# Performance work log

Measured on AMD Instinct MI355X. Metric: run time of the kernel, lower is better.

## Reference

```python
import jax, jax.numpy as jnp
import numpy as np

B, N, C, H = 4, 1025, 768, 12
KEEP_RATIO = 0.25
BETA = 1.0


def setup_inputs() -> dict:
    key = jax.random.key(0)
    k1, k2, k3, k4, k5 = jax.random.split(key, 5)
    x = jax.random.normal(k1, (B, N, C), dtype=jnp.float32)
    ucb_count_score = jax.random.uniform(k2, (H, N), dtype=jnp.float32)
    W_qkv = jax.random.normal(k3, (C, 3 * C), dtype=jnp.float32) * 0.02
    W_proj = jax.random.normal(k4, (C, C), dtype=jnp.float32) * 0.02
    b_proj = jax.random.normal(k5, (C,), dtype=jnp.float32) * 0.02
    return {"x": x, "ucb_count_score": ucb_count_score, "W_qkv": W_qkv,
            "W_proj": W_proj, "b_proj": b_proj, "counter": 100, "ucb_enabled": 1}


def reference(x, ucb_count_score, W_qkv, W_proj, b_proj, counter, ucb_enabled):
    Bn, Nn, Cn = x.shape
    Dh = Cn // H
    scale = Dh ** -0.5
    # qkv projection (no bias, qkv_bias=False)
    qkv = (x @ W_qkv).reshape(Bn, Nn, 3, H, Dh)
    q = jnp.transpose(qkv[:, :, 0], (0, 2, 1, 3))  # [B,H,N,Dh]
    k = jnp.transpose(qkv[:, :, 1], (0, 2, 1, 3))
    v = jnp.transpose(qkv[:, :, 2], (0, 2, 1, 3))
    attn_probs = jax.nn.softmax(jnp.einsum('bhnd,bhmd->bhnm', q, k) * scale, axis=-1)

    if ucb_enabled and counter > 50:
        # UCB pruning path (exclude_cls=True, keep_ratio set)
        total_patches = Nn - 1
        k_sel = max(1, int(total_patches * KEEP_RATIO))
        patch_scores = attn_probs[:, :, :, 1:].mean(axis=2)  # [B,H,N-1]
        expl = BETA * jnp.sqrt(jnp.log(counter + 1.0) / (ucb_count_score[:, 1:] + 1e-6))  # [H,N-1]
        global_ucb = (patch_scores + expl[None]).mean(axis=1)  # [B,N-1]
        _, sel = jax.lax.top_k(global_ucb, k_sel)  # [B,k]
        tok = sel + 1  # shift for CLS
        # keep[b,j] = 1 if token j is CLS or selected in batch b
        keep = jnp.zeros((Bn, Nn), dtype=attn_probs.dtype)
        keep = keep.at[jnp.arange(Bn)[:, None], tok].set(1.0).at[:, 0].set(1.0)
        # mask[b,h,i,j] = keep[b,i] OR keep[b,j]
        mask = jnp.maximum(keep[:, None, :, None], keep[:, None, None, :])
        pruned = attn_probs * mask
        pruned = pruned / (pruned.sum(axis=-1, keepdims=True) + 1e-8)
        context = jnp.einsum('bhnm,bhmd->bhnd', pruned, v)
        cnt = jnp.zeros((Nn,), dtype=jnp.float32).at[tok.reshape(-1)].add(1.0) / Bn
        score_delta = jnp.broadcast_to(cnt[None, :], ucb_count_score.shape)
    else:
        context = jnp.einsum('bhnm,bhmd->bhnd', attn_probs, v)
        score_delta = None

    out = context.transpose(0, 2, 1, 3).reshape(Bn, Nn, Cn) @ W_proj + b_proj
    return out, score_delta
```

## Files before the change

kernel.cpp:

```cpp
#include <hip/hip_runtime.h>
#include <hip/hip_bf16.h>
#include <math.h>

#define Bb 4
#define Nn 1025
#define Cc 768
#define Hh 12
#define BH (Bb*Hh)
#define M_ROWS 4100
#define KSEL 256
#define JP 1152
#define IT_TILES 68
#define NIB 17
#define NIB32 33
#define NSW 9
#define MT16 264
#define KC24 24
#define JT16 72
#define JT32 36
#define STR4 292
#define NPART 396
#define NSCORE 1024
#define QSCALE 0.18033688011112042f

#define CAST_X_BLK 1584
#define CAST_WQKV_BLK 864
#define CAST_WPROJ_BLK 288

typedef __attribute__((ext_vector_type(8))) short short8;
typedef __attribute__((ext_vector_type(4))) short short4s;
typedef __attribute__((ext_vector_type(4))) float floatx4;
typedef __attribute__((ext_vector_type(4))) unsigned uintx4;

static __device__ inline unsigned short f2bf(float v) {
    __hip_bfloat16 b = __float2bfloat16(v);
    return *reinterpret_cast<unsigned short*>(&b);
}
static __device__ inline float fexp2(float x) {
    return __builtin_amdgcn_exp2f(x);
}
static __device__ inline unsigned pkbf(float lo, float hi) {
    union { float f; unsigned u; } a, b;
    a.f = lo; b.f = hi;
    return (a.u >> 16) | (b.u & 0xffff0000u);
}

static __device__ inline void async16(const unsigned short* g, unsigned short* l) {
    __builtin_amdgcn_global_load_lds(
        (const __attribute__((address_space(1))) unsigned int*)g,
        (__attribute__((address_space(3))) unsigned int*)l, 16, 0, 0);
}

__global__ __launch_bounds__(256)
void cast_all(const float* __restrict__ x, const float* __restrict__ Wqkv,
              const float* __restrict__ Wproj,
              unsigned short* __restrict__ xA, unsigned short* __restrict__ WB,
              unsigned short* __restrict__ WpB)
{
    int blk = blockIdx.x;
    int tid = threadIdx.x;
    if (blk < CAST_X_BLK) {
        int s = blk * 256 + tid;
        int ml = s & 15, q = (s >> 4) & 3;
        int t2 = s >> 6;
        int mt = t2 % MT16, kc = t2 / MT16;
        int m = mt * 16 + ml, k = kc * 32 + q * 8;
        uint4 pk = {0u, 0u, 0u, 0u};
        if (m < M_ROWS) {
            float4 a = *(const float4*)&x[(size_t)m * 768 + k];
            float4 b2 = *(const float4*)&x[(size_t)m * 768 + k + 4];
            pk.x = (unsigned)f2bf(a.x)  | ((unsigned)f2bf(a.y)  << 16);
            pk.y = (unsigned)f2bf(a.z)  | ((unsigned)f2bf(a.w)  << 16);
            pk.z = (unsigned)f2bf(b2.x) | ((unsigned)f2bf(b2.y) << 16);
            pk.w = (unsigned)f2bf(b2.z) | ((unsigned)f2bf(b2.w) << 16);
        }
        *(uint4*)&xA[(size_t)s * 8] = pk;
        return;
    }
    const float* W;
    unsigned short* WO;
    int N, NT, s;
    if (blk < CAST_X_BLK + CAST_WQKV_BLK) {
        W = Wqkv; WO = WB; N = 2304; NT = 144;
        s = (blk - CAST_X_BLK) * 256 + tid;
    } else {
        W = Wproj; WO = WpB; N = 768; NT = 48;
        s = (blk - CAST_X_BLK - CAST_WQKV_BLK) * 256 + tid;
    }
    int nl = s & 15, q = (s >> 4) & 3;
    int t2 = s >> 6;
    int nt = t2 % NT, kc = t2 / NT;
    int n = nt * 16 + nl, k = kc * 32 + q * 8;
    unsigned hv[8];
#pragma unroll
    for (int e = 0; e < 8; ++e)
        hv[e] = f2bf(W[(size_t)(k + e) * N + n]);
    uint4 pk;
    pk.x = hv[0] | (hv[1] << 16);
    pk.y = hv[2] | (hv[3] << 16);
    pk.z = hv[4] | (hv[5] << 16);
    pk.w = hv[6] | (hv[7] << 16);
    *(uint4*)&WO[(size_t)s * 8] = pk;
}

template<int NT, int MODE>
__global__ __launch_bounds__(256, 3)
void gemm_mfma(const unsigned short* __restrict__ Af,
               const unsigned short* __restrict__ Bf,
               int Nt16,
               unsigned short* __restrict__ qB, unsigned short* __restrict__ kF,
               unsigned short* __restrict__ vF,
               float* __restrict__ outp, const float* __restrict__ bias)
{
    __shared__ __align__(16) unsigned short ldsA[4096];
    __shared__ __align__(16) unsigned short ldsB[NT * 1024];
    const int tid = threadIdx.x;
    const int ln = tid & 63, w = tid >> 6;
    const int wm = w >> 1, wn = w & 1;
    const int mb = blockIdx.x, nb = blockIdx.y;

    floatx4 acc[4][NT];
#pragma unroll
    for (int mt = 0; mt < 4; ++mt)
#pragma unroll
        for (int nt = 0; nt < NT; ++nt)
            acc[mt][nt] = (floatx4){0.f, 0.f, 0.f, 0.f};

    for (int kc = 0; kc < KC24; ++kc) {
        const unsigned short* gA = Af + ((size_t)(kc * MT16 + mb * 8)) * 512;
        const unsigned short* gB = Bf + ((size_t)(kc * Nt16 + nb * (NT * 2))) * 512;
        async16(gA + (size_t)(w * 128 + ln) * 8,      &ldsA[w * 1024]);
        async16(gA + (size_t)(w * 128 + 64 + ln) * 8, &ldsA[w * 1024 + 512]);
        if (NT == 4) {
            async16(gB + (size_t)(w * 128 + ln) * 8,      &ldsB[w * 1024]);
            async16(gB + (size_t)(w * 128 + 64 + ln) * 8, &ldsB[w * 1024 + 512]);
        } else {
            async16(gB + (size_t)(w * 64 + ln) * 8, &ldsB[w * 512]);
        }
        __syncthreads();

        short8 Am[4], Bn[NT];
#pragma unroll
        for (int mt = 0; mt < 4; ++mt)
            Am[mt] = *(const short8*)&ldsA[((wm * 4 + mt) * 64 + ln) * 8];
#pragma unroll
        for (int nt = 0; nt < NT; ++nt)
            Bn[nt] = *(const short8*)&ldsB[((wn * NT + nt) * 64 + ln) * 8];
#pragma unroll
        for (int mt = 0; mt < 4; ++mt)
#pragma unroll
            for (int nt = 0; nt < NT; ++nt)
                acc[mt][nt] = __builtin_amdgcn_mfma_f32_16x16x32_bf16(
                    Am[mt], Bn[nt], acc[mt][nt], 0, 0, 0);
        __syncthreads();
    }

    const int q = ln >> 4, l15 = ln & 15;
    if (MODE == 1) {
#pragma unroll
        for (int nt = 0; nt < NT; ++nt) {
            int gn = nb * (NT * 32) + wn * (NT * 16) + nt * 16 + l15;
            float bv = bias[gn];
#pragma unroll
            for (int mt = 0; mt < 4; ++mt) {
                int gmb = mb * 128 + wm * 64 + mt * 16 + q * 4;
#pragma unroll
                for (int r = 0; r < 4; ++r) {
                    int gm = gmb + r;
                    if (gm < M_ROWS)
                        outp[(size_t)gm * 768 + gn] = acc[mt][nt][r] + bv;
                }
            }
        }
    } else {
#pragma unroll
        for (int nt = 0; nt < NT; ++nt) {
            int gn = nb * (NT * 32) + wn * (NT * 16) + nt * 16 + l15;
            int s = (gn >= 1536) ? 2 : (gn >= 768 ? 1 : 0);
            int rr = gn - s * Cc;
            int h = rr >> 6, d = rr & 63;
#pragma unroll
            for (int mt = 0; mt < 4; ++mt) {
                int gmb = mb * 128 + wm * 64 + mt * 16 + q * 4;
#pragma unroll
                for (int r = 0; r < 4; ++r) {
                    int gm = gmb + r;
                    if (gm >= M_ROWS) continue;
                    int b = gm / Nn;
                    int n = gm - b * Nn;
                    int bh = b * Hh + h;
                    float val = acc[mt][nt][r];
                    if (s == 0) {
                        int idx = (((bh * IT_TILES + (n >> 4)) * 2 + (d >> 5)) * 512)
                                  + ((((d & 31) >> 3) * 16 + (n & 15)) * 8) + (d & 7);
                        qB[idx] = f2bf(val * QSCALE);
                    } else if (s == 1) {
                        size_t idx = ((((size_t)bh * JT16 + (n >> 4)) * 2 + (d >> 5)) * 64
                                      + ((d >> 3) & 3) * 16 + (n & 15)) * 8 + (d & 7);
                        kF[idx] = f2bf(val);
                    } else {
                        size_t idx = ((((size_t)bh * JT32 + (n >> 5)) * 4 + (d >> 4)) * 64
                                      + ((n >> 3) & 3) * 16 + (d & 15)) * 8 + (n & 7);
                        vF[idx] = f2bf(val);
                    }
                }
            }
        }
    }
}

__global__ __launch_bounds__(256, 4)
void attn_colsum_mfma(const unsigned short* __restrict__ qB,
                      const unsigned short* __restrict__ kF,
                      float* __restrict__ colsum_part)
{
    __shared__ unsigned int expS8[32 * STR4];
    __shared__ float red16[16][32];
    __shared__ float linv[32];

    const int blk = blockIdx.x;
    const int x8 = blk & 7, g = blk >> 3;
    const int bh = x8 * 6 + (g % 6);
    const int ib = g / 6;
    const int tid = threadIdx.x;
    const int ws = tid >> 6;
    const int ln = tid & 63;
    const int i16 = ln & 15, q = ln >> 4;

    const unsigned short* kBase = kF + (size_t)bh * JT16 * 1024;

    short8 Qf[2][2];
#pragma unroll
    for (int it = 0; it < 2; ++it)
#pragma unroll
        for (int kc = 0; kc < 2; ++kc)
            Qf[it][kc] = *(const short8*)&qB[(((size_t)bh * IT_TILES + ib * 2 + it) * 2 + kc) * 512 + ln * 8];

    float lacc[2][2] = {{0.f, 0.f}, {0.f, 0.f}};

    short8 Kc[2][2], Kn[2][2];
#pragma unroll
    for (int jt = 0; jt < 2; ++jt)
#pragma unroll
        for (int kc = 0; kc < 2; ++kc)
            Kc[jt][kc] = *(const short8*)&kBase[(((ws * 2 + jt) * 2 + kc) * 64 + ln) * 8];

    for (int sw = 0; sw < NSW; ++sw) {
        if (sw + 1 < NSW) {
#pragma unroll
            for (int jt = 0; jt < 2; ++jt)
#pragma unroll
                for (int kc = 0; kc < 2; ++kc)
                    Kn[jt][kc] = *(const short8*)&kBase[((((sw + 1) * 8 + ws * 2 + jt) * 2 + kc) * 64 + ln) * 8];
        }

        floatx4 S[2][2];
#pragma unroll
        for (int it = 0; it < 2; ++it)
#pragma unroll
            for (int jt = 0; jt < 2; ++jt) {
                S[it][jt] = (floatx4){0.f, 0.f, 0.f, 0.f};
#pragma unroll
                for (int kc = 0; kc < 2; ++kc)
                    S[it][jt] = __builtin_amdgcn_mfma_f32_16x16x32_bf16(Kc[jt][kc], Qf[it][kc], S[it][jt], 0, 0, 0);
            }

        const int jbase0 = sw * 128 + ws * 32 + q * 4;
#pragma unroll
        for (int it = 0; it < 2; ++it) {
            const int irow = it * 16 + i16;
#pragma unroll
            for (int jt = 0; jt < 2; ++jt) {
                int jbase = jbase0 + jt * 16;
                float p[4];
#pragma unroll
                for (int r = 0; r < 4; ++r) {
                    float vld = (jbase + r < Nn) ? 1.f : 0.f;
                    p[r] = fexp2(S[it][jt][r]) * vld;
                }
                lacc[it][jt] += (p[0] + p[1]) + (p[2] + p[3]);
                unsigned u = (unsigned)__builtin_amdgcn_cvt_pk_fp8_f32(p[0], p[1], 0, false);
                u = (unsigned)__builtin_amdgcn_cvt_pk_fp8_f32(p[2], p[3], (int)u, true);
                expS8[irow * STR4 + (jbase >> 2)] = u;
            }
        }
#pragma unroll
        for (int jt = 0; jt < 2; ++jt)
#pragma unroll
            for (int kc = 0; kc < 2; ++kc)
                Kc[jt][kc] = Kn[jt][kc];
    }

    __syncthreads();
#pragma unroll
    for (int it = 0; it < 2; ++it)
        red16[ws * 4 + q][it * 16 + i16] = lacc[it][0] + lacc[it][1];
    __syncthreads();
    if (tid < 32) {
        float s = 0.f;
#pragma unroll
        for (int t = 0; t < 16; ++t) s += red16[t][tid];
        int gi = ib * 32 + tid;
        linv[tid] = (gi < Nn) ? 1.f / s : 0.f;
    }
    __syncthreads();

    float* prow = colsum_part + (size_t)(bh * NIB32 + ib) * JP;
    for (int grp = tid; grp < 288; grp += 256) {
        float a0 = 0.f, a1 = 0.f, a2 = 0.f, a3 = 0.f;
#pragma unroll 8
        for (int i = 0; i < 32; ++i) {
            unsigned v = expS8[i * STR4 + grp];
            float li = linv[i];
            a0 += __builtin_amdgcn_cvt_f32_fp8(v, 0) * li;
            a1 += __builtin_amdgcn_cvt_f32_fp8(v, 1) * li;
            a2 += __builtin_amdgcn_cvt_f32_fp8(v, 2) * li;
            a3 += __builtin_amdgcn_cvt_f32_fp8(v, 3) * li;
        }
        float4 o = {a0, a1, a2, a3};
        *(float4*)&prow[grp * 4] = o;
    }
}

__global__ __launch_bounds__(256)
void colsum_reduce(const float* __restrict__ colsum_part,
                   const float* __restrict__ ucb_score,
                   const int* __restrict__ counter_p,
                   float* __restrict__ scoreF)
{
    const int b = blockIdx.x, jc = blockIdx.y;
    const int tid = threadIdx.x;
    const int j32 = tid & 31, grp = tid >> 5;
    const int t = jc * 32 + j32 + 1;
    __shared__ float red[8][32];

    const float* pb = colsum_part + (size_t)b * NPART * JP + t;
    float a0 = 0.f, a1 = 0.f;
    int r = grp;
    for (; r + 8 < NPART; r += 16) {
        a0 += pb[(size_t)r * JP];
        a1 += pb[(size_t)(r + 8) * JP];
    }
    for (; r < NPART; r += 8) a0 += pb[(size_t)r * JP];
    red[grp][j32] = a0 + a1;
    __syncthreads();

    if (tid < 32) {
        float cs = 0.f;
#pragma unroll
        for (int g = 0; g < 8; ++g) cs += red[g][tid];
        int tt = jc * 32 + tid + 1;
        float lc = logf((float)(*counter_p) + 1.0f);
        float s = cs * (1.0f / (float)Nn);
#pragma unroll
        for (int h = 0; h < Hh; ++h)
            s += sqrtf(lc / (ucb_score[h * Nn + tt] + 1e-6f));
        s *= (1.0f / (float)Hh);
        scoreF[b * NSCORE + tt - 1] = s;
    }
}

__global__ __launch_bounds__(1024)
void ucb_topk(const float* __restrict__ scoreF,
              float* __restrict__ keepP, float* __restrict__ cnt_b)
{
    const int b = blockIdx.x;
    const int tid = threadIdx.x;
    const int w = tid >> 6, ln = tid & 63;
    __shared__ int hist[8192];
    __shared__ int wtot[16];
    __shared__ unsigned ckey[1024];
    __shared__ int cidx[1024];
    __shared__ int s_tb, s_rem, ccount;

    for (int tpos = tid; tpos < JP; tpos += 1024) {
        keepP[b * JP + tpos] = 0.f;
        cnt_b[b * JP + tpos] = 0.f;
    }

    const unsigned key = __float_as_uint(scoreF[b * NSCORE + tid]);

    for (int tpos = tid; tpos < 8192; tpos += 1024) hist[tpos] = 0;
    if (tid == 0) ccount = 0;
    __syncthreads();
    atomicAdd(&hist[key >> 18], 1);
    __syncthreads();

    int part = 0;
#pragma unroll
    for (int q2 = 0; q2 < 8; ++q2) part += hist[tid * 8 + q2];
    int v = part;
#pragma unroll
    for (int off = 1; off < 64; off <<= 1) {
        int tv = __shfl_down(v, off);
        if (ln + off < 64) v += tv;
    }
    if (ln == 0) wtot[w] = v;
    __syncthreads();
    int woff = 0;
    for (int w2 = w + 1; w2 < 16; ++w2) woff += wtot[w2];
    int cum_above = v + woff - part;
    for (int q2 = 7; q2 >= 0; --q2) {
        int c = hist[tid * 8 + q2];
        if (cum_above < KSEL && cum_above + c >= KSEL) {
            s_tb = tid * 8 + q2;
            s_rem = KSEL - cum_above;
        }
        cum_above += c;
    }
    __syncthreads();

    const int tb = s_tb, rem = s_rem;
    const int mybin = (int)(key >> 18);
    bool sel = mybin > tb;
    if (mybin == tb) {
        int p = atomicAdd(&ccount, 1);
        ckey[p] = key; cidx[p] = tid;
    }
    __syncthreads();
    if (mybin == tb) {
        int rr = 0;
        const int cc = ccount;
        for (int c = 0; c < cc; ++c) {
            unsigned kc2 = ckey[c]; int ic = cidx[c];
            if (kc2 > key || (kc2 == key && ic < tid)) ++rr;
        }
        sel = rr < rem;
    }
    if (sel) {
        int tok = tid + 1;
        keepP[b * JP + tok] = 1.f;
        cnt_b[b * JP + tok] = 1.0f / (float)Bb;
    }
    if (tid == 0) keepP[b * JP + 0] = 1.f;
}

__global__ __launch_bounds__(256, 2)
void attn_ctx_mfma(const unsigned short* __restrict__ qB,
                   const unsigned short* __restrict__ kF,
                   const unsigned short* __restrict__ vF,
                   const float* __restrict__ keepP, const float* __restrict__ cnt_b,
                   unsigned short* __restrict__ ctxA, float* __restrict__ out2)
{
    __shared__ __align__(16) char smem[25856];
    float* keeps = (float*)smem;
    float* red16 = (float*)(smem + 4608);
    float* dinv  = (float*)(smem + 8704);
    float* redC  = (float*)(smem + 8960);

    const int blk = blockIdx.x;
    const int x8 = blk & 7, g = blk >> 3;
    const int bh = x8 * 6 + (g % 6);
    const int ib = g / 6;
    const int b = bh / Hh, h = bh % Hh;
    const int tid = threadIdx.x;
    const int ws = tid >> 6;
    const int ln = tid & 63;
    const int i16 = ln & 15, q = ln >> 4;

    {
        int t = blk * 256 + tid;
        if (t < Hh * Nn) {
            int n = t % Nn;
            out2[t] = cnt_b[0 * JP + n] + cnt_b[1 * JP + n]
                    + cnt_b[2 * JP + n] + cnt_b[3 * JP + n];
        }
    }

    for (int t = tid; t < JP; t += 256) keeps[t] = keepP[b * JP + t];

    const unsigned short* kBase = kF + (size_t)bh * JT16 * 1024;
    const unsigned short* vBase = vF + (size_t)bh * JT32 * 2048;

    short8 Qf[4][2];
#pragma unroll
    for (int it = 0; it < 4; ++it)
#pragma unroll
        for (int kc = 0; kc < 2; ++kc)
            Qf[it][kc] = *(const short8*)&qB[(((size_t)bh * IT_TILES + ib * 4 + it) * 2 + kc) * 512 + ln * 8];

    __syncthreads();

    float keepi[4];
#pragma unroll
    for (int it = 0; it < 4; ++it)
        keepi[it] = keeps[(ib * 4 + it) * 16 + i16];

    floatx4 ctxacc[4][4];
#pragma unroll
    for (int it = 0; it < 4; ++it)
#pragma unroll
        for (int dt = 0; dt < 4; ++dt)
            ctxacc[it][dt] = (floatx4){0.f, 0.f, 0.f, 0.f};
    float dsacc[4] = {0.f, 0.f, 0.f, 0.f};

    short8 Kc[2][2], Kn[2][2];
    short8 Vc8[4], Vn8[4];
#pragma unroll
    for (int jt = 0; jt < 2; ++jt)
#pragma unroll
        for (int kc = 0; kc < 2; ++kc)
            Kc[jt][kc] = *(const short8*)&kBase[(((ws * 2 + jt) * 2 + kc) * 64 + ln) * 8];
#pragma unroll
    for (int dt = 0; dt < 4; ++dt)
        Vc8[dt] = *(const short8*)&vBase[(((size_t)ws * 4 + dt) * 64 + ln) * 8];

    for (int sw = 0; sw < NSW; ++sw) {
        if (sw + 1 < NSW) {
#pragma unroll
            for (int jt = 0; jt < 2; ++jt)
#pragma unroll
                for (int kc = 0; kc < 2; ++kc)
                    Kn[jt][kc] = *(const short8*)&kBase[((((sw + 1) * 8 + ws * 2 + jt) * 2 + kc) * 64 + ln) * 8];
#pragma unroll
            for (int dt = 0; dt < 4; ++dt)
                Vn8[dt] = *(const short8*)&vBase[((((size_t)(sw + 1) * 4 + ws) * 4 + dt) * 64 + ln) * 8];
        }

        float kjv[2][4], vld[2][4];
#pragma unroll
        for (int jt = 0; jt < 2; ++jt)
#pragma unroll
            for (int r = 0; r < 4; ++r) {
                int jj = sw * 128 + ws * 32 + jt * 16 + q * 4 + r;
                vld[jt][r] = (jj < Nn) ? 1.f : 0.f;
                kjv[jt][r] = keeps[jj];
            }

#pragma unroll
        for (int it = 0; it < 4; ++it) {
            floatx4 S[2];
#pragma unroll
            for (int jt = 0; jt < 2; ++jt) {
                S[jt] = (floatx4){0.f, 0.f, 0.f, 0.f};
#pragma unroll
                for (int kc = 0; kc < 2; ++kc)
                    S[jt] = __builtin_amdgcn_mfma_f32_16x16x32_bf16(Kc[jt][kc], Qf[it][kc], S[jt], 0, 0, 0);
            }
            bool rk = keepi[it] > 0.5f;
            float p[2][4];
#pragma unroll
            for (int jt = 0; jt < 2; ++jt)
#pragma unroll
                for (int r = 0; r < 4; ++r) {
                    float w = rk ? vld[jt][r] : kjv[jt][r];
                    p[jt][r] = fexp2(S[jt][r]) * w;
                    dsacc[it] += p[jt][r];
                }
            unsigned Au = pkbf(p[0][0], p[0][1]);
            unsigned Bu = pkbf(p[0][2], p[0][3]);
            unsigned Cu = pkbf(p[1][0], p[1][1]);
            unsigned Du = pkbf(p[1][2], p[1][3]);
            asm("v_permlane32_swap_b32 %0, %1" : "+v"(Au), "+v"(Cu));
            asm("v_permlane32_swap_b32 %0, %1" : "+v"(Bu), "+v"(Du));
            asm("v_permlane16_swap_b32 %0, %1" : "+v"(Au), "+v"(Cu));
            asm("v_permlane16_swap_b32 %0, %1" : "+v"(Bu), "+v"(Du));
            short8 Wf = __builtin_bit_cast(short8, (uintx4){Au, Bu, Cu, Du});
#pragma unroll
            for (int dt = 0; dt < 4; ++dt)
                ctxacc[it][dt] = __builtin_amdgcn_mfma_f32_16x16x32_bf16(
                    Wf, Vc8[dt], ctxacc[it][dt], 0, 0, 0);
        }

#pragma unroll
        for (int jt = 0; jt < 2; ++jt)
#pragma unroll
            for (int kc = 0; kc < 2; ++kc)
                Kc[jt][kc] = Kn[jt][kc];
#pragma unroll
        for (int dt = 0; dt < 4; ++dt)
            Vc8[dt] = Vn8[dt];
    }

    __syncthreads();
#pragma unroll
    for (int it = 0; it < 4; ++it) red16[(ws * 4 + q) * 64 + it * 16 + i16] = dsacc[it];
    __syncthreads();
    if (tid < 64) {
        float s = 0.f;
#pragma unroll
        for (int t = 0; t < 16; ++t) s += red16[t * 64 + tid];
        dinv[tid] = 1.f / (s + 1e-8f);
    }
    for (int w = 0; w < 4; ++w) {
        __syncthreads();
        if (ws == w) {
#pragma unroll
            for (int it = 0; it < 4; ++it)
#pragma unroll
                for (int dt = 0; dt < 4; ++dt)
#pragma unroll
                    for (int r = 0; r < 4; ++r) {
                        int i = it * 16 + q * 4 + r;
                        int d = dt * 16 + i16;
                        float v = ctxacc[it][dt][r];
                        redC[i * 66 + d] = (w == 0) ? v : (redC[i * 66 + d] + v);
                    }
        }
    }
    __syncthreads();
#pragma unroll
    for (int rep = 0; rep < 2; ++rep) {
        int s2 = tid + rep * 256;
        int i = s2 >> 3, dc = s2 & 7;
        int gi = ib * 64 + i;
        if (gi < Nn) {
            int m = b * Nn + gi;
            float dv = dinv[i];
            const float* src = &redC[i * 66 + dc * 8];
            uint4 pk;
            pk.x = (unsigned)f2bf(src[0] * dv) | ((unsigned)f2bf(src[1] * dv) << 16);
            pk.y = (unsigned)f2bf(src[2] * dv) | ((unsigned)f2bf(src[3] * dv) << 16);
            pk.z = (unsigned)f2bf(src[4] * dv) | ((unsigned)f2bf(src[5] * dv) << 16);
            pk.w = (unsigned)f2bf(src[6] * dv) | ((unsigned)f2bf(src[7] * dv) << 16);
            int kc2 = h * 2 + (dc >> 2);
            int q2 = dc & 3;
            size_t idx = (((size_t)(kc2 * MT16 + (m >> 4))) * 64 + q2 * 16 + (m & 15)) * 8;
            *(uint4*)&ctxA[idx] = pk;
        }
    }
}

extern "C" void kernel_launch(void* const* d_in, const int* in_sizes, int n_in,
                              void* d_out, int out_size, void* d_ws, size_t ws_size,
                              hipStream_t stream) {
    const float* x     = (const float*)d_in[0];
    const float* ucb   = (const float*)d_in[1];
    const float* Wqkv  = (const float*)d_in[2];
    const float* Wproj = (const float*)d_in[3];
    const float* bproj = (const float*)d_in[4];
    const int*   counter = (const int*)d_in[5];

    unsigned short* qB = (unsigned short*)d_ws;
    unsigned short* kF = qB + 3342336;
    unsigned short* vF = kF + 3538944;
    float* keepP    = (float*)(vF + 3538944);
    float* cnt_b    = keepP + 4608;
    unsigned short* ctxA = (unsigned short*)(cnt_b + 4608);
    unsigned short* xA   = ctxA + 3244032;
    unsigned short* WB   = xA + 3244032;
    unsigned short* WpB  = WB + 1769472;
    float* colsum_part = (float*)(WpB + 589824);
    float* scoreF = colsum_part + 1824768;

    float* out  = (float*)d_out;
    float* out2 = out + 3148800;

    cast_all<<<dim3(CAST_X_BLK + CAST_WQKV_BLK + CAST_WPROJ_BLK), dim3(256), 0, stream>>>(
        x, Wqkv, Wproj, xA, WB, WpB);
    gemm_mfma<4, 0><<<dim3(33, 18), dim3(256), 0, stream>>>(
        xA, WB, 144, qB, kF, vF, nullptr, nullptr);
    attn_colsum_mfma<<<dim3(8 * 198), dim3(256), 0, stream>>>(qB, kF, colsum_part);
    colsum_reduce<<<dim3(Bb, 32), dim3(256), 0, stream>>>(colsum_part, ucb, counter, scoreF);
    ucb_topk<<<dim3(Bb), dim3(1024), 0, stream>>>(scoreF, keepP, cnt_b);
    attn_ctx_mfma<<<dim3(8 * 102), dim3(256), 0, stream>>>(qB, kF, vF, keepP, cnt_b, ctxA, out2);
    gemm_mfma<2, 1><<<dim3(33, 12), dim3(256), 0, stream>>>(
        ctxA, WpB, 48, nullptr, nullptr, nullptr, out, bproj);
}
```

Baseline: 201.1 us.

## Split context attention into kept-row and pruned-row passes over gathered kept tokens

After top-k, the kernel builds a compact list of kept token indices and adds a gather kernel that packs the kept Q, K and V tiles into contiguous buffers. The context kernel is split in two. Kept query rows attend over all keys. Non-kept query rows attend only over the gathered kept keys, about 257 instead of 1025. This removes the masked exp/MFMA work that the old dense pass did for pruned key columns, at the cost of an extra gather launch, scattered element-wise V gathers and more launch/indexing complexity.

```diff
diff --git a/kernel.cpp b/kernel.cpp
--- a/kernel.cpp
+++ b/kernel.cpp
@@ -11,7 +11,6 @@
 #define KSEL 256
 #define JP 1152
 #define IT_TILES 68
-#define NIB 17
 #define NIB32 33
 #define NSW 9
 #define MT16 264
@@ -21,6 +20,9 @@
 #define STR4 292
 #define NPART 396
 #define NSCORE 1024
+#define KT 17
+#define KGT 18
+#define KVG 9
 #define QSCALE 0.18033688011112042f
 
 #define CAST_X_BLK 1584
@@ -28,7 +30,6 @@
 #define CAST_WPROJ_BLK 288
 
 typedef __attribute__((ext_vector_type(8))) short short8;
-typedef __attribute__((ext_vector_type(4))) short short4s;
 typedef __attribute__((ext_vector_type(4))) float floatx4;
 typedef __attribute__((ext_vector_type(4))) unsigned uintx4;
 
@@ -362,13 +363,15 @@
 
 __global__ __launch_bounds__(1024)
 void ucb_topk(const float* __restrict__ scoreF,
-              float* __restrict__ keepP, float* __restrict__ cnt_b)
+              float* __restrict__ keepP, float* __restrict__ cnt_b,
+              int* __restrict__ keptIdx)
 {
     const int b = blockIdx.x;
     const int tid = threadIdx.x;
     const int w = tid >> 6, ln = tid & 63;
     __shared__ int hist[8192];
     __shared__ int wtot[16];
+    __shared__ int wcnt[16];
     __shared__ unsigned ckey[1024];
     __shared__ int cidx[1024];
     __shared__ int s_tb, s_rem, ccount;
@@ -377,6 +380,8 @@
         keepP[b * JP + tpos] = 0.f;
         cnt_b[b * JP + tpos] = 0.f;
     }
+    for (int tpos = tid; tpos < KT * 16 + 16; tpos += 1024)
+        keptIdx[b * (KT * 16 + 16) + tpos] = -1;
 
     const unsigned key = __float_as_uint(scoreF[b * NSCORE + tid]);
 
@@ -433,30 +438,86 @@
         cnt_b[b * JP + tok] = 1.0f / (float)Bb;
     }
     if (tid == 0) keepP[b * JP + 0] = 1.f;
-}
-
-__global__ __launch_bounds__(256, 2)
-void attn_ctx_mfma(const unsigned short* __restrict__ qB,
-                   const unsigned short* __restrict__ kF,
-                   const unsigned short* __restrict__ vF,
-                   const float* __restrict__ keepP, const float* __restrict__ cnt_b,
-                   unsigned short* __restrict__ ctxA, float* __restrict__ out2)
+
+    unsigned long long m = __ballot(sel);
+    int rk = (int)__popcll(m & ((1ull << ln) - 1ull));
+    if (ln == 0) wcnt[w] = (int)__popcll(m);
+    __syncthreads();
+    int off2 = 1;
+    for (int w2 = 0; w2 < w; ++w2) off2 += wcnt[w2];
+    if (sel) keptIdx[b * (KT * 16 + 16) + off2 + rk] = tid + 1;
+    if (tid == 0) keptIdx[b * (KT * 16 + 16) + 0] = 0;
+}
+
+__global__ __launch_bounds__(256)
+void gather_kv(const unsigned short* __restrict__ qB, const unsigned short* __restrict__ kF,
+               const unsigned short* __restrict__ vF, const int* __restrict__ keptIdx,
+               unsigned short* __restrict__ qG, unsigned short* __restrict__ kG,
+               unsigned short* __restrict__ vG)
 {
-    __shared__ __align__(16) char smem[25856];
-    float* keeps = (float*)smem;
-    float* red16 = (float*)(smem + 4608);
-    float* dinv  = (float*)(smem + 8704);
-    float* redC  = (float*)(smem + 8960);
+    const int blk = blockIdx.x, tid = threadIdx.x;
+    const int KIS = KT * 16 + 16;
+    if (blk < 408) {
+        int sid = blk * 256 + tid;
+        int lane = sid & 63, kc = (sid >> 6) & 1;
+        int t = (sid >> 7) % KT, bh = (sid >> 7) / KT;
+        int np = t * 16 + (lane & 15), lh = lane >> 4, b = bh / Hh;
+        int src = keptIdx[b * KIS + np];
+        uint4 v = {0u, 0u, 0u, 0u};
+        if (src >= 0)
+            v = *(const uint4*)&qB[((((size_t)bh * IT_TILES + (src >> 4)) * 2 + kc) * 64
+                                    + lh * 16 + (src & 15)) * 8];
+        *(uint4*)&qG[((((size_t)bh * KT + t) * 2 + kc) * 64 + lane) * 8] = v;
+    } else if (blk < 816) {
+        int sid = (blk - 408) * 256 + tid;
+        int lane = sid & 63, kc = (sid >> 6) & 1;
+        int t = (sid >> 7) % KT, bh = (sid >> 7) / KT;
+        int jp = t * 16 + (lane & 15), lh = lane >> 4, b = bh / Hh;
+        int src = keptIdx[b * KIS + jp];
+        uint4 v = {0u, 0u, 0u, 0u};
+        if (src >= 0)
+            v = *(const uint4*)&kF[((((size_t)bh * JT16 + (src >> 4)) * 2 + kc) * 64
+                                    + lh * 16 + (src & 15)) * 8];
+        *(uint4*)&kG[((((size_t)bh * KGT + t) * 2 + kc) * 64 + lane) * 8] = v;
+    } else {
+        int sid = (blk - 816) * 256 + tid;
+        int lane = sid & 63, dt = (sid >> 6) & 3;
+        int g = (sid >> 8) % KVG, bh = (sid >> 8) / KVG, b = bh / Hh;
+        unsigned short vv[8];
+#pragma unroll
+        for (int e = 0; e < 8; ++e) {
+            int jp = g * 32 + (lane >> 4) * 8 + e;
+            int src = keptIdx[b * KIS + jp];
+            vv[e] = 0;
+            if (src >= 0)
+                vv[e] = vF[((((size_t)bh * JT32 + (src >> 5)) * 4 + dt) * 64
+                            + ((src >> 3) & 3) * 16 + (lane & 15)) * 8 + (src & 7)];
+        }
+        *(uint4*)&vG[((((size_t)bh * KVG + g) * 4 + dt) * 64 + lane) * 8] =
+            *(uint4*)vv;
+    }
+}
+
+__global__ __launch_bounds__(256, 3)
+void attn_ctx_split(const unsigned short* __restrict__ qB,
+                    const unsigned short* __restrict__ qG,
+                    const unsigned short* __restrict__ kF,
+                    const unsigned short* __restrict__ kG,
+                    const unsigned short* __restrict__ vF,
+                    const unsigned short* __restrict__ vG,
+                    const float* __restrict__ keepP, const float* __restrict__ cnt_b,
+                    const int* __restrict__ keptIdx,
+                    unsigned short* __restrict__ ctxA, float* __restrict__ out2)
+{
+    __shared__ float ctxs[4][16][66];
+    __shared__ float wden[4][16];
 
     const int blk = blockIdx.x;
-    const int x8 = blk & 7, g = blk >> 3;
-    const int bh = x8 * 6 + (g % 6);
-    const int ib = g / 6;
-    const int b = bh / Hh, h = bh % Hh;
+    const int x8 = blk & 7, g0 = blk >> 3;
     const int tid = threadIdx.x;
-    const int ws = tid >> 6;
-    const int ln = tid & 63;
+    const int ws = tid >> 6, ln = tid & 63;
     const int i16 = ln & 15, q = ln >> 4;
+    const int KIS = KT * 16 + 16;
 
     {
         int t = blk * 256 + tid;
@@ -467,152 +528,145 @@
         }
     }
 
-    for (int t = tid; t < JP; t += 256) keeps[t] = keepP[b * JP + t];
-
-    const unsigned short* kBase = kF + (size_t)bh * JT16 * 1024;
-    const unsigned short* vBase = vF + (size_t)bh * JT32 * 2048;
-
-    short8 Qf[4][2];
-#pragma unroll
-    for (int it = 0; it < 4; ++it)
+    const bool isK2 = (g0 < 30);
+    int bh, rtile, NG;
+    const unsigned short *qSrc, *kSrc, *vSrc;
+    if (isK2) {
+        int gg = g0;
+        bh = x8 * 6 + (gg % 6);
+        int rb = gg / 6;
+        rtile = rb * 4 + ws;
+        if (rtile >= KT) return;
+        NG = 33;
+        qSrc = qG + (((size_t)bh * KT + rtile) * 2) * 512;
+        kSrc = kF + (size_t)bh * JT16 * 1024;
+        vSrc = vF + (size_t)bh * JT32 * 2048;
+    } else {
+        int gg = g0 - 30;
+        bh = x8 * 6 + (gg % 6);
+        int ib = gg / 6;
+        rtile = ib * 4 + ws;
+        NG = 9;
+        qSrc = qB + (((size_t)bh * IT_TILES + rtile) * 2) * 512;
+        kSrc = kG + (size_t)bh * KGT * 1024;
+        vSrc = vG + (size_t)bh * KVG * 2048;
+    }
+    const int b = bh / Hh, h = bh % Hh;
+
+    short8 Qf[2];
+#pragma unroll
+    for (int kc = 0; kc < 2; ++kc)
+        Qf[kc] = *(const short8*)&qSrc[kc * 512 + ln * 8];
+
+    floatx4 acc[4];
+#pragma unroll
+    for (int dt = 0; dt < 4; ++dt) acc[dt] = (floatx4){0.f, 0.f, 0.f, 0.f};
+    float dsacc = 0.f;
+
+    short8 Kc[2][2], Kn[2][2], Vc[4], Vn[4];
+#pragma unroll
+    for (int j2 = 0; j2 < 2; ++j2)
 #pragma unroll
         for (int kc = 0; kc < 2; ++kc)
-            Qf[it][kc] = *(const short8*)&qB[(((size_t)bh * IT_TILES + ib * 4 + it) * 2 + kc) * 512 + ln * 8];
-
-    __syncthreads();
-
-    float keepi[4];
-#pragma unroll
-    for (int it = 0; it < 4; ++it)
-        keepi[it] = keeps[(ib * 4 + it) * 16 + i16];
-
-    floatx4 ctxacc[4][4];
-#pragma unroll
-    for (int it = 0; it < 4; ++it)
+            Kc[j2][kc] = *(const short8*)&kSrc[(size_t)j2 * 1024 + kc * 512 + ln * 8];
+#pragma unroll
+    for (int dt = 0; dt < 4; ++dt)
+        Vc[dt] = *(const short8*)&vSrc[(size_t)dt * 512 + ln * 8];
+
+    for (int g = 0; g < NG - 1; ++g) {
+#pragma unroll
+        for (int j2 = 0; j2 < 2; ++j2)
+#pragma unroll
+            for (int kc = 0; kc < 2; ++kc)
+                Kn[j2][kc] = *(const short8*)&kSrc[((size_t)(2 * g + 2 + j2)) * 1024 + kc * 512 + ln * 8];
 #pragma unroll
         for (int dt = 0; dt < 4; ++dt)
-            ctxacc[it][dt] = (floatx4){0.f, 0.f, 0.f, 0.f};
-    float dsacc[4] = {0.f, 0.f, 0.f, 0.f};
-
-    short8 Kc[2][2], Kn[2][2];
-    short8 Vc8[4], Vn8[4];
-#pragma unroll
-    for (int jt = 0; jt < 2; ++jt)
+            Vn[dt] = *(const short8*)&vSrc[((size_t)(g + 1)) * 2048 + dt * 512 + ln * 8];
+
+        floatx4 S0 = (floatx4){0.f, 0.f, 0.f, 0.f};
+        floatx4 S1 = (floatx4){0.f, 0.f, 0.f, 0.f};
+#pragma unroll
+        for (int kc = 0; kc < 2; ++kc) {
+            S0 = __builtin_amdgcn_mfma_f32_16x16x32_bf16(Kc[0][kc], Qf[kc], S0, 0, 0, 0);
+            S1 = __builtin_amdgcn_mfma_f32_16x16x32_bf16(Kc[1][kc], Qf[kc], S1, 0, 0, 0);
+        }
+        float p0[4], p1[4];
+#pragma unroll
+        for (int r = 0; r < 4; ++r) {
+            p0[r] = fexp2(S0[r]);
+            p1[r] = fexp2(S1[r]);
+        }
+        dsacc += ((p0[0] + p0[1]) + (p0[2] + p0[3]))
+               + ((p1[0] + p1[1]) + (p1[2] + p1[3]));
+        unsigned Au = pkbf(p0[0], p0[1]), Bu = pkbf(p0[2], p0[3]);
+        unsigned Cu = pkbf(p1[0], p1[1]), Du = pkbf(p1[2], p1[3]);
+        asm("v_permlane32_swap_b32 %0, %1" : "+v"(Au), "+v"(Cu));
+        asm("v_permlane32_swap_b32 %0, %1" : "+v"(Bu), "+v"(Du));
+        asm("v_permlane16_swap_b32 %0, %1" : "+v"(Au), "+v"(Cu));
+        asm("v_permlane16_swap_b32 %0, %1" : "+v"(Bu), "+v"(Du));
+        short8 Wf = __builtin_bit_cast(short8, (uintx4){Au, Bu, Cu, Du});
+#pragma unroll
+        for (int dt = 0; dt < 4; ++dt)
+            acc[dt] = __builtin_amdgcn_mfma_f32_16x16x32_bf16(Wf, Vc[dt], acc[dt], 0, 0, 0);
+
+#pragma unroll
+        for (int j2 = 0; j2 < 2; ++j2)
+#pragma unroll
+            for (int kc = 0; kc < 2; ++kc)
+                Kc[j2][kc] = Kn[j2][kc];
+#pragma unroll
+        for (int dt = 0; dt < 4; ++dt)
+            Vc[dt] = Vn[dt];
+    }
+
+    {
+        floatx4 S0 = (floatx4){0.f, 0.f, 0.f, 0.f};
 #pragma unroll
         for (int kc = 0; kc < 2; ++kc)
-            Kc[jt][kc] = *(const short8*)&kBase[(((ws * 2 + jt) * 2 + kc) * 64 + ln) * 8];
+            S0 = __builtin_amdgcn_mfma_f32_16x16x32_bf16(Kc[0][kc], Qf[kc], S0, 0, 0, 0);
+        float pv = (q == 0) ? fexp2(S0[0]) : 0.f;
+        dsacc += pv;
+        unsigned Au = pkbf(pv, 0.f), Bu = 0u, Cu = 0u, Du = 0u;
+        asm("v_permlane32_swap_b32 %0, %1" : "+v"(Au), "+v"(Cu));
+        asm("v_permlane32_swap_b32 %0, %1" : "+v"(Bu), "+v"(Du));
+        asm("v_permlane16_swap_b32 %0, %1" : "+v"(Au), "+v"(Cu));
+        asm("v_permlane16_swap_b32 %0, %1" : "+v"(Bu), "+v"(Du));
+        short8 Wf = __builtin_bit_cast(short8, (uintx4){Au, Bu, Cu, Du});
+#pragma unroll
+        for (int dt = 0; dt < 4; ++dt)
+            acc[dt] = __builtin_amdgcn_mfma_f32_16x16x32_bf16(Wf, Vc[dt], acc[dt], 0, 0, 0);
+    }
+
+    float d1 = dsacc + __shfl_xor(dsacc, 16);
+    float dden = d1 + __shfl_xor(d1, 32);
+    if (q == 0) wden[ws][i16] = dden;
+
 #pragma unroll
     for (int dt = 0; dt < 4; ++dt)
-        Vc8[dt] = *(const short8*)&vBase[(((size_t)ws * 4 + dt) * 64 + ln) * 8];
-
-    for (int sw = 0; sw < NSW; ++sw) {
-        if (sw + 1 < NSW) {
-#pragma unroll
-            for (int jt = 0; jt < 2; ++jt)
-#pragma unroll
-                for (int kc = 0; kc < 2; ++kc)
-                    Kn[jt][kc] = *(const short8*)&kBase[((((sw + 1) * 8 + ws * 2 + jt) * 2 + kc) * 64 + ln) * 8];
-#pragma unroll
-            for (int dt = 0; dt < 4; ++dt)
-                Vn8[dt] = *(const short8*)&vBase[((((size_t)(sw + 1) * 4 + ws) * 4 + dt) * 64 + ln) * 8];
-        }
-
-        float kjv[2][4], vld[2][4];
-#pragma unroll
-        for (int jt = 0; jt < 2; ++jt)
-#pragma unroll
-            for (int r = 0; r < 4; ++r) {
-                int jj = sw * 128 + ws * 32 + jt * 16 + q * 4 + r;
-                vld[jt][r] = (jj < Nn) ? 1.f : 0.f;
-                kjv[jt][r] = keeps[jj];
-            }
-
-#pragma unroll
-        for (int it = 0; it < 4; ++it) {
-            floatx4 S[2];
-#pragma unroll
-            for (int jt = 0; jt < 2; ++jt) {
-                S[jt] = (floatx4){0.f, 0.f, 0.f, 0.f};
-#pragma unroll
-                for (int kc = 0; kc < 2; ++kc)
-                    S[jt] = __builtin_amdgcn_mfma_f32_16x16x32_bf16(Kc[jt][kc], Qf[it][kc], S[jt], 0, 0, 0);
-            }
-            bool rk = keepi[it] > 0.5f;
-            float p[2][4];
-#pragma unroll
-            for (int jt = 0; jt < 2; ++jt)
-#pragma unroll
-                for (int r = 0; r < 4; ++r) {
-                    float w = rk ? vld[jt][r] : kjv[jt][r];
-                    p[jt][r] = fexp2(S[jt][r]) * w;
-                    dsacc[it] += p[jt][r];
-                }
-            unsigned Au = pkbf(p[0][0], p[0][1]);
-            unsigned Bu = pkbf(p[0][2], p[0][3]);
-            unsigned Cu = pkbf(p[1][0], p[1][1]);
-            unsigned Du = pkbf(p[1][2], p[1][3]);
-            asm("v_permlane32_swap_b32 %0, %1" : "+v"(Au), "+v"(Cu));
-            asm("v_permlane32_swap_b32 %0, %1" : "+v"(Bu), "+v"(Du));
-            asm("v_permlane16_swap_b32 %0, %1" : "+v"(Au), "+v"(Cu));
-            asm("v_permlane16_swap_b32 %0, %1" : "+v"(Bu), "+v"(Du));
-            short8 Wf = __builtin_bit_cast(short8, (uintx4){Au, Bu, Cu, Du});
-#pragma unroll
-            for (int dt = 0; dt < 4; ++dt)
-                ctxacc[it][dt] = __builtin_amdgcn_mfma_f32_16x16x32_bf16(
-                    Wf, Vc8[dt], ctxacc[it][dt], 0, 0, 0);
-        }
-
-#pragma unroll
-        for (int jt = 0; jt < 2; ++jt)
-#pragma unroll
-            for (int kc = 0; kc < 2; ++kc)
-                Kc[jt][kc] = Kn[jt][kc];
-#pragma unroll
-        for (int dt = 0; dt < 4; ++dt)
-            Vc8[dt] = Vn8[dt];
-    }
-
-    __syncthreads();
-#pragma unroll
-    for (int it = 0; it < 4; ++it) red16[(ws * 4 + q) * 64 + it * 16 + i16] = dsacc[it];
-    __syncthreads();
-    if (tid < 64) {
-        float s = 0.f;
-#pragma unroll
-        for (int t = 0; t < 16; ++t) s += red16[t * 64 + tid];
-        dinv[tid] = 1.f / (s + 1e-8f);
-    }
-    for (int w = 0; w < 4; ++w) {
-        __syncthreads();
-        if (ws == w) {
-#pragma unroll
-            for (int it = 0; it < 4; ++it)
-#pragma unroll
-                for (int dt = 0; dt < 4; ++dt)
-#pragma unroll
-                    for (int r = 0; r < 4; ++r) {
-                        int i = it * 16 + q * 4 + r;
-                        int d = dt * 16 + i16;
-                        float v = ctxacc[it][dt][r];
-                        redC[i * 66 + d] = (w == 0) ? v : (redC[i * 66 + d] + v);
-                    }
-        }
-    }
-    __syncthreads();
-#pragma unroll
-    for (int rep = 0; rep < 2; ++rep) {
-        int s2 = tid + rep * 256;
-        int i = s2 >> 3, dc = s2 & 7;
-        int gi = ib * 64 + i;
-        if (gi < Nn) {
-            int m = b * Nn + gi;
-            float dv = dinv[i];
-            const float* src = &redC[i * 66 + dc * 8];
+#pragma unroll
+        for (int r = 0; r < 4; ++r)
+            ctxs[ws][q * 4 + r][dt * 16 + i16] = acc[dt][r];
+
+#pragma unroll
+    for (int round = 0; round < 2; ++round) {
+        int s2 = ln + round * 64;
+        int row = s2 >> 3, dc = s2 & 7;
+        int m = -1;
+        if (isK2) {
+            int src = keptIdx[b * KIS + rtile * 16 + row];
+            if (src >= 0) m = b * Nn + src;
+        } else {
+            int gi = rtile * 16 + row;
+            if (gi < Nn && keepP[b * JP + gi] < 0.5f) m = b * Nn + gi;
+        }
+        if (m >= 0) {
+            float dv = 1.f / (wden[ws][row] + 1e-8f);
+            const float* src8 = &ctxs[ws][row][dc * 8];
             uint4 pk;
-            pk.x = (unsigned)f2bf(src[0] * dv) | ((unsigned)f2bf(src[1] * dv) << 16);
-            pk.y = (unsigned)f2bf(src[2] * dv) | ((unsigned)f2bf(src[3] * dv) << 16);
-            pk.z = (unsigned)f2bf(src[4] * dv) | ((unsigned)f2bf(src[5] * dv) << 16);
-            pk.w = (unsigned)f2bf(src[6] * dv) | ((unsigned)f2bf(src[7] * dv) << 16);
+            pk.x = (unsigned)f2bf(src8[0] * dv) | ((unsigned)f2bf(src8[1] * dv) << 16);
+            pk.y = (unsigned)f2bf(src8[2] * dv) | ((unsigned)f2bf(src8[3] * dv) << 16);
+            pk.z = (unsigned)f2bf(src8[4] * dv) | ((unsigned)f2bf(src8[5] * dv) << 16);
+            pk.w = (unsigned)f2bf(src8[6] * dv) | ((unsigned)f2bf(src8[7] * dv) << 16);
             int kc2 = h * 2 + (dc >> 2);
             int q2 = dc & 3;
             size_t idx = (((size_t)(kc2 * MT16 + (m >> 4))) * 64 + q2 * 16 + (m & 15)) * 8;
@@ -642,6 +696,10 @@
     unsigned short* WpB  = WB + 1769472;
     float* colsum_part = (float*)(WpB + 589824);
     float* scoreF = colsum_part + 1824768;
+    int* keptIdx  = (int*)(scoreF + 4096);
+    unsigned short* qG = (unsigned short*)(keptIdx + 1152);
+    unsigned short* kG = qG + 835584;
+    unsigned short* vG = kG + 884736;
 
     float* out  = (float*)d_out;
     float* out2 = out + 3148800;
@@ -652,8 +710,10 @@
         xA, WB, 144, qB, kF, vF, nullptr, nullptr);
     attn_colsum_mfma<<<dim3(8 * 198), dim3(256), 0, stream>>>(qB, kF, colsum_part);
     colsum_reduce<<<dim3(Bb, 32), dim3(256), 0, stream>>>(colsum_part, ucb, counter, scoreF);
-    ucb_topk<<<dim3(Bb), dim3(1024), 0, stream>>>(scoreF, keepP, cnt_b);
-    attn_ctx_mfma<<<dim3(8 * 102), dim3(256), 0, stream>>>(qB, kF, vF, keepP, cnt_b, ctxA, out2);
+    ucb_topk<<<dim3(Bb), dim3(1024), 0, stream>>>(scoreF, keepP, cnt_b, keptIdx);
+    gather_kv<<<dim3(1248), dim3(256), 0, stream>>>(qB, kF, vF, keptIdx, qG, kG, vG);
+    attn_ctx_split<<<dim3(8 * 132), dim3(256), 0, stream>>>(
+        qB, qG, kF, kG, vF, vG, keepP, cnt_b, keptIdx, ctxA, out2);
     gemm_mfma<2, 1><<<dim3(33, 12), dim3(256), 0, stream>>>(
         ctxA, WpB, 48, nullptr, nullptr, nullptr, out, bproj);
 }
```

New measurement: 205.8 us. 1.02x slower.
